# Optimization experiments

Measured on AMD Instinct MI355X. Metric: run time of the kernel, lower is better.

Reference implementation:

```python
import jax, jax.numpy as jnp
import numpy as np

IN_F = 8192
OUT_F = 8192
TOKENS = 4096
QP = 127.0   # 2**(8-1) - 1
QN = -128.0  # -2**(8-1)


def setup_inputs() -> dict:
    key = jax.random.key(0)
    k1, k2 = jax.random.split(key)
    x = jax.random.normal(k1, (TOKENS, IN_F), dtype=jnp.float32)
    # torch.randint(0, 2, ...) -> values in {0, 1}
    weight = jax.random.randint(k2, (OUT_F, IN_F), 0, 2, dtype=jnp.int32)
    weight_scale = jnp.ones((1,), dtype=jnp.float32)
    bias = jnp.zeros((OUT_F,), dtype=jnp.float32)
    return {"x": x, "weight": weight, "weight_scale": weight_scale, "bias": bias}


def reference(x, weight, weight_scale, bias):
    # activation_quant: per-row symmetric int8 quantization
    s = QP / jnp.clip(jnp.max(jnp.abs(x), axis=-1, keepdims=True), 1e-5)  # [T,1]
    x_q = jnp.clip(jnp.round(x * s), QN, QP)  # int8 values held in f32 (exact)
    y = jnp.einsum('tk,nk->tn', x_q, weight.astype(x.dtype))  # [T, OUT_F]
    # post_quant_process: dequantize by activation scale then weight scale
    out = y / s / weight_scale
    return out + bias[None, :]
```

## Files before the change

### kernel.cpp

```cpp
#include <hip/hip_runtime.h>

#define TOKENS 4096
#define IN_F   8192
#define OUT_F  8192

typedef int v4i __attribute__((ext_vector_type(4)));

__device__ __forceinline__ void gload_lds16(const void* g, void* l) {
    __builtin_amdgcn_global_load_lds(
        (const __attribute__((address_space(1))) void*)g,
        (__attribute__((address_space(3))) void*)l, 16, 0, 0);
}

__global__ __launch_bounds__(256) void quant_kernel(const float* __restrict__ x,
                                                    signed char* __restrict__ xq,
                                                    float* __restrict__ recip_s) {
    const int row = blockIdx.x;
    const int t   = threadIdx.x;
    const float4* xr = (const float4*)(x + (size_t)row * IN_F);
    float4 v[8];
    float m = 0.f;
#pragma unroll
    for (int i = 0; i < 8; ++i) {
        v[i] = xr[t + 256 * i];
        m = fmaxf(m, fmaxf(fmaxf(fabsf(v[i].x), fabsf(v[i].y)),
                           fmaxf(fabsf(v[i].z), fabsf(v[i].w))));
    }
#pragma unroll
    for (int off = 32; off > 0; off >>= 1)
        m = fmaxf(m, __shfl_xor(m, off));
    __shared__ float wmax[4];
    if ((t & 63) == 0) wmax[t >> 6] = m;
    __syncthreads();
    m = fmaxf(fmaxf(wmax[0], wmax[1]), fmaxf(wmax[2], wmax[3]));
    m = fmaxf(m, 1e-5f);
    const float s = 127.0f / m;
    if (t == 0) recip_s[row] = m / 127.0f;
    unsigned int* out = (unsigned int*)(xq + (size_t)row * IN_F);
#pragma unroll
    for (int i = 0; i < 8; ++i) {
        int a = (int)fminf(fmaxf(rintf(v[i].x * s), -128.f), 127.f);
        int b = (int)fminf(fmaxf(rintf(v[i].y * s), -128.f), 127.f);
        int c = (int)fminf(fmaxf(rintf(v[i].z * s), -128.f), 127.f);
        int d = (int)fminf(fmaxf(rintf(v[i].w * s), -128.f), 127.f);
        out[t + 256 * i] = (a & 255) | ((b & 255) << 8) | ((c & 255) << 16) | ((d & 255) << 24);
    }
}

__global__ __launch_bounds__(256) void pack_w(const int* __restrict__ w,
                                              unsigned int* __restrict__ w8) {
    const size_t idx = (size_t)blockIdx.x * 256 + threadIdx.x;
    int4 a = ((const int4*)w)[idx];
    w8[idx] = (a.x & 255) | ((a.y & 255) << 8) | ((a.z & 255) << 16) | ((a.w & 255) << 24);
}

__global__ __launch_bounds__(256, 2) void gemm_kernel(const signed char* __restrict__ A,
                                                      const signed char* __restrict__ B,
                                                      const float* __restrict__ recip_s,
                                                      const float* __restrict__ wscale,
                                                      const float* __restrict__ bias,
                                                      float* __restrict__ out) {
    __shared__ signed char As[128 * 64];
    __shared__ signed char Bs[256 * 64];
    const int t    = threadIdx.x;
    const int wave = t >> 6;
    const int lane = t & 63;
    const int m0 = blockIdx.y * 128;
    const int n0 = blockIdx.x * 256;
    const int wm = (wave >> 1) * 64;
    const int wn = (wave & 1) * 128;

    v4i acc[4][8] = {};

    const int rowS = t >> 2;
    const int colS = ((t & 3) ^ ((t >> 3) & 3)) * 16;
    const signed char* gA = A + (size_t)(m0 + rowS) * IN_F + colS;
    const signed char* gB = B + (size_t)(n0 + rowS) * IN_F + colS;
    signed char* lA = As + t * 16;
    signed char* lB = Bs + t * 16;

    const int r16 = lane & 15;
    const int q   = lane >> 4;
    const int cOff = ((q ^ ((r16 >> 1) & 3)) * 16);

    for (int k0 = 0; k0 < IN_F; k0 += 64) {
        gload_lds16(gA + k0, lA);
        gload_lds16(gA + (size_t)64 * IN_F + k0, lA + 4096);
        gload_lds16(gB + k0, lB);
        gload_lds16(gB + (size_t)64 * IN_F + k0, lB + 4096);
        gload_lds16(gB + (size_t)128 * IN_F + k0, lB + 8192);
        gload_lds16(gB + (size_t)192 * IN_F + k0, lB + 12288);
        __syncthreads();

        v4i a[4], b[8];
#pragma unroll
        for (int i = 0; i < 4; ++i)
            a[i] = *(const v4i*)(As + (wm + i * 16 + r16) * 64 + cOff);
#pragma unroll
        for (int j = 0; j < 8; ++j)
            b[j] = *(const v4i*)(Bs + (wn + j * 16 + r16) * 64 + cOff);
#pragma unroll
        for (int i = 0; i < 4; ++i)
#pragma unroll
            for (int j = 0; j < 8; ++j)
                acc[i][j] = __builtin_amdgcn_mfma_i32_16x16x64_i8(a[i], b[j], acc[i][j], 0, 0, 0);
        __syncthreads();
    }

    const float rws = 1.0f / wscale[0];
#pragma unroll
    for (int i = 0; i < 4; ++i) {
#pragma unroll
        for (int r = 0; r < 4; ++r) {
            const int row = m0 + wm + i * 16 + q * 4 + r;
            const float rs = recip_s[row] * rws;
#pragma unroll
            for (int j = 0; j < 8; ++j) {
                const int col = n0 + wn + j * 16 + r16;
                out[(size_t)row * OUT_F + col] = (float)acc[i][j][r] * rs + bias[col];
            }
        }
    }
}

extern "C" void kernel_launch(void* const* d_in, const int* in_sizes, int n_in,
                              void* d_out, int out_size, void* d_ws, size_t ws_size,
                              hipStream_t stream) {
    const float* x      = (const float*)d_in[0];
    const int*   w      = (const int*)d_in[1];
    const float* wscale = (const float*)d_in[2];
    const float* bias   = (const float*)d_in[3];
    float* out = (float*)d_out;

    signed char* xq = (signed char*)d_ws;
    signed char* w8 = xq + (size_t)TOKENS * IN_F;
    float* recip_s  = (float*)(w8 + (size_t)OUT_F * IN_F);

    quant_kernel<<<TOKENS, 256, 0, stream>>>(x, xq, recip_s);
    pack_w<<<(int)(((size_t)OUT_F * IN_F) / 4 / 256), 256, 0, stream>>>(w, (unsigned int*)w8);
    dim3 grid(OUT_F / 256, TOKENS / 128);
    gemm_kernel<<<grid, 256, 0, stream>>>(xq, w8, recip_s, wscale, bias, out);
}
```

Measured before the change: 736.4 us.

## Double-buffer LDS tiles in int8 GEMM to overlap global loads with MFMA

Doubles the A and B shared-memory tiles and prefetches the next K-slice with global_load_lds before computing on the current one. The trailing barrier in the K loop is dropped, leaving one barrier per iteration. The aim is to hide global-to-LDS load latency behind MFMA work. In exchange, LDS use per block doubles, and the overlap can be lost if the compiler makes the LDS reads wait on the outstanding direct-to-LDS loads.

```diff
diff --git a/kernel.cpp b/kernel.cpp
--- a/kernel.cpp
+++ b/kernel.cpp
@@ -60,8 +60,8 @@
                                                       const float* __restrict__ wscale,
                                                       const float* __restrict__ bias,
                                                       float* __restrict__ out) {
-    __shared__ signed char As[128 * 64];
-    __shared__ signed char Bs[256 * 64];
+    __shared__ signed char As[2 * 128 * 64];
+    __shared__ signed char Bs[2 * 256 * 64];
     const int t    = threadIdx.x;
     const int wave = t >> 6;
     const int lane = t & 63;
@@ -83,28 +83,47 @@
     const int q   = lane >> 4;
     const int cOff = ((q ^ ((r16 >> 1) & 3)) * 16);
 
+    gload_lds16(gA, lA);
+    gload_lds16(gA + (size_t)64 * IN_F, lA + 4096);
+    gload_lds16(gB, lB);
+    gload_lds16(gB + (size_t)64 * IN_F, lB + 4096);
+    gload_lds16(gB + (size_t)128 * IN_F, lB + 8192);
+    gload_lds16(gB + (size_t)192 * IN_F, lB + 12288);
+
+    int buf = 0;
     for (int k0 = 0; k0 < IN_F; k0 += 64) {
-        gload_lds16(gA + k0, lA);
-        gload_lds16(gA + (size_t)64 * IN_F + k0, lA + 4096);
-        gload_lds16(gB + k0, lB);
-        gload_lds16(gB + (size_t)64 * IN_F + k0, lB + 4096);
-        gload_lds16(gB + (size_t)128 * IN_F + k0, lB + 8192);
-        gload_lds16(gB + (size_t)192 * IN_F + k0, lB + 12288);
         __syncthreads();
 
+        const int kn = k0 + 64;
+        if (kn < IN_F) {
+            const int nb = (buf ^ 1) * 4096 * 2;
+            signed char* nA = lA + (buf ^ 1) * 8192;
+            signed char* nB = lB + (buf ^ 1) * 16384;
+            gload_lds16(gA + kn, nA);
+            gload_lds16(gA + (size_t)64 * IN_F + kn, nA + 4096);
+            gload_lds16(gB + kn, nB);
+            gload_lds16(gB + (size_t)64 * IN_F + kn, nB + 4096);
+            gload_lds16(gB + (size_t)128 * IN_F + kn, nB + 8192);
+            gload_lds16(gB + (size_t)192 * IN_F + kn, nB + 12288);
+            (void)nb;
+        }
+
+        const signed char* pA = As + buf * 8192;
+        const signed char* pB = Bs + buf * 16384;
         v4i a[4], b[8];
 #pragma unroll
         for (int i = 0; i < 4; ++i)
-            a[i] = *(const v4i*)(As + (wm + i * 16 + r16) * 64 + cOff);
+            a[i] = *(const v4i*)(pA + (wm + i * 16 + r16) * 64 + cOff);
 #pragma unroll
         for (int j = 0; j < 8; ++j)
-            b[j] = *(const v4i*)(Bs + (wn + j * 16 + r16) * 64 + cOff);
+            b[j] = *(const v4i*)(pB + (wn + j * 16 + r16) * 64 + cOff);
 #pragma unroll
         for (int i = 0; i < 4; ++i)
 #pragma unroll
             for (int j = 0; j < 8; ++j)
                 acc[i][j] = __builtin_amdgcn_mfma_i32_16x16x64_i8(a[i], b[j], acc[i][j], 0, 0, 0);
-        __syncthreads();
+
+        buf ^= 1;
     }
 
     const float rws = 1.0f / wscale[0];
```

Result: slower. 765.2 us (+3.9%).

## Double-buffer LDS tiles and switch GEMM to 32x32x32 i8 MFMA

Applied to the files above, without the earlier changes.

Rewrites the int8 GEMM main loop to double-buffer the A/B tiles in LDS, prefetching the next K-slice with direct global-to-LDS loads while MFMAs run on the current one, with one barrier per iteration. It also switches from 16x16x64 to 32x32x32 int8 MFMA with a new fragment-friendly LDS layout that needs no XOR swizzle, and splits register fragment reads into two K-halves to overlap LDS reads with math. LDS use doubles, which may reduce occupancy, and the epilogue is remapped to the 32x32 accumulator layout.

```diff
diff --git a/kernel.cpp b/kernel.cpp
--- a/kernel.cpp
+++ b/kernel.cpp
@@ -4,7 +4,8 @@
 #define IN_F   8192
 #define OUT_F  8192
 
-typedef int v4i __attribute__((ext_vector_type(4)));
+typedef int v4i  __attribute__((ext_vector_type(4)));
+typedef int v16i __attribute__((ext_vector_type(16)));
 
 __device__ __forceinline__ void gload_lds16(const void* g, void* l) {
     __builtin_amdgcn_global_load_lds(
@@ -60,67 +61,100 @@
                                                       const float* __restrict__ wscale,
                                                       const float* __restrict__ bias,
                                                       float* __restrict__ out) {
-    __shared__ signed char As[128 * 64];
-    __shared__ signed char Bs[256 * 64];
+    __shared__ signed char As[2 * 8192];
+    __shared__ signed char Bs[2 * 16384];
     const int t    = threadIdx.x;
     const int wave = t >> 6;
     const int lane = t & 63;
     const int m0 = blockIdx.y * 128;
     const int n0 = blockIdx.x * 256;
-    const int wm = (wave >> 1) * 64;
-    const int wn = (wave & 1) * 128;
+    const int wmHalf = wave >> 1;
+    const int wnHalf = wave & 1;
 
-    v4i acc[4][8] = {};
+    v16i acc[2][4] = {};
 
-    const int rowS = t >> 2;
-    const int colS = ((t & 3) ^ ((t >> 3) & 3)) * 16;
-    const signed char* gA = A + (size_t)(m0 + rowS) * IN_F + colS;
-    const signed char* gB = B + (size_t)(n0 + rowS) * IN_F + colS;
+    const int rowOff = ((t >> 7) & 1) * 32 + (t & 31);
+    const int kOff   = ((t >> 6) & 1) * 32 + ((t >> 5) & 1) * 16;
+    const signed char* gA = A + (size_t)(m0 + rowOff) * IN_F + kOff;
+    const signed char* gB = B + (size_t)(n0 + rowOff) * IN_F + kOff;
     signed char* lA = As + t * 16;
     signed char* lB = Bs + t * 16;
 
-    const int r16 = lane & 15;
-    const int q   = lane >> 4;
-    const int cOff = ((q ^ ((r16 >> 1) & 3)) * 16);
+    const signed char* aBase = As + wmHalf * 4096 + lane * 16;
+    const signed char* bBase = Bs + wnHalf * 8192 + lane * 16;
 
-    for (int k0 = 0; k0 < IN_F; k0 += 64) {
-        gload_lds16(gA + k0, lA);
-        gload_lds16(gA + (size_t)64 * IN_F + k0, lA + 4096);
-        gload_lds16(gB + k0, lB);
-        gload_lds16(gB + (size_t)64 * IN_F + k0, lB + 4096);
-        gload_lds16(gB + (size_t)128 * IN_F + k0, lB + 8192);
-        gload_lds16(gB + (size_t)192 * IN_F + k0, lB + 12288);
-        __syncthreads();
+#define STAGE(KC, BSEL) do {                                          \
+        signed char* dA = lA + (BSEL) * 8192;                         \
+        signed char* dB = lB + (BSEL) * 16384;                        \
+        gload_lds16(gA + (size_t)(KC), dA);                           \
+        gload_lds16(gA + (size_t)64 * IN_F + (KC), dA + 4096);        \
+        gload_lds16(gB + (size_t)(KC), dB);                           \
+        gload_lds16(gB + (size_t)64 * IN_F + (KC), dB + 4096);       \
+        gload_lds16(gB + (size_t)128 * IN_F + (KC), dB + 8192);      \
+        gload_lds16(gB + (size_t)192 * IN_F + (KC), dB + 12288);     \
+    } while (0)
 
-        v4i a[4], b[8];
-#pragma unroll
-        for (int i = 0; i < 4; ++i)
-            a[i] = *(const v4i*)(As + (wm + i * 16 + r16) * 64 + cOff);
-#pragma unroll
-        for (int j = 0; j < 8; ++j)
-            b[j] = *(const v4i*)(Bs + (wn + j * 16 + r16) * 64 + cOff);
-#pragma unroll
-        for (int i = 0; i < 4; ++i)
-#pragma unroll
-            for (int j = 0; j < 8; ++j)
-                acc[i][j] = __builtin_amdgcn_mfma_i32_16x16x64_i8(a[i], b[j], acc[i][j], 0, 0, 0);
-        __syncthreads();
+#define READ_FRAGS(AV, BV, BSEL, KS) do {                                             \
+        _Pragma("unroll")                                                             \
+        for (int i = 0; i < 2; ++i)                                                   \
+            AV[i] = *(const v4i*)(aBase + (BSEL) * 8192 + i * 2048 + (KS) * 1024);    \
+        _Pragma("unroll")                                                             \
+        for (int j = 0; j < 4; ++j)                                                   \
+            BV[j] = *(const v4i*)(bBase + (BSEL) * 16384 + j * 2048 + (KS) * 1024);   \
+    } while (0)
+
+#define DO_MFMA(AV, BV) do {                                                          \
+        _Pragma("unroll")                                                             \
+        for (int i = 0; i < 2; ++i)                                                   \
+            _Pragma("unroll")                                                         \
+            for (int j = 0; j < 4; ++j)                                               \
+                acc[i][j] = __builtin_amdgcn_mfma_i32_32x32x32_i8(AV[i], BV[j],       \
+                                                                  acc[i][j], 0, 0, 0);\
+    } while (0)
+
+    v4i a0[2], b0[4], a1[2], b1[4];
+
+    STAGE(0, 0);
+    asm volatile("s_waitcnt vmcnt(0)" ::: "memory");
+    asm volatile("s_barrier" ::: "memory");
+    READ_FRAGS(a0, b0, 0, 0);
+    STAGE(64, 1);
+
+    int buf = 0;
+    for (int k0 = 0; k0 < IN_F - 64; k0 += 64) {
+        READ_FRAGS(a1, b1, buf, 1);
+        DO_MFMA(a0, b0);
+        asm volatile("s_waitcnt vmcnt(0) lgkmcnt(0)" ::: "memory");
+        asm volatile("s_barrier" ::: "memory");
+        READ_FRAGS(a0, b0, buf ^ 1, 0);
+        if (k0 + 128 < IN_F) STAGE(k0 + 128, buf);
+        DO_MFMA(a1, b1);
+        buf ^= 1;
     }
+    READ_FRAGS(a1, b1, buf, 1);
+    DO_MFMA(a0, b0);
+    DO_MFMA(a1, b1);
 
     const float rws = 1.0f / wscale[0];
+    const int rl = lane & 31;
+    const int q  = lane >> 5;
+    const int colBase = n0 + wnHalf * 128 + rl;
 #pragma unroll
-    for (int i = 0; i < 4; ++i) {
+    for (int i = 0; i < 2; ++i) {
 #pragma unroll
-        for (int r = 0; r < 4; ++r) {
-            const int row = m0 + wm + i * 16 + q * 4 + r;
+        for (int reg = 0; reg < 16; ++reg) {
+            const int row = m0 + wmHalf * 64 + i * 32 + (reg & 3) + 8 * (reg >> 2) + 4 * q;
             const float rs = recip_s[row] * rws;
 #pragma unroll
-            for (int j = 0; j < 8; ++j) {
-                const int col = n0 + wn + j * 16 + r16;
-                out[(size_t)row * OUT_F + col] = (float)acc[i][j][r] * rs + bias[col];
+            for (int j = 0; j < 4; ++j) {
+                const int col = colBase + j * 32;
+                out[(size_t)row * OUT_F + col] = (float)acc[i][j][reg] * rs + bias[col];
             }
         }
     }
+#undef STAGE
+#undef READ_FRAGS
+#undef DO_MFMA
 }
 
 extern "C" void kernel_launch(void* const* d_in, const int* in_sizes, int n_in,
```

After: 845.7 us. 1.15x slower.
